# Optimization experiments

Measured on AMD Instinct MI355X. Metric: run time of the kernel, lower is better.

## Reference

```python
import jax, jax.numpy as jnp
import numpy as np

CONTEXT_LENGTH = 4096
INPUT_LENGTH = 1024
N_EMBED = 512
HEAD_SIZE = 64
BATCH = 8


def _prefix_causal_mask(T):
    # A=ones(IL,IL), B=zeros(IL,non), C=ones(non,IL), D=tril(non,non)
    il = INPUT_LENGTH
    non = CONTEXT_LENGTH - il
    top = jnp.concatenate([jnp.ones((il, il)), jnp.zeros((il, non))], axis=1)
    bot = jnp.concatenate([jnp.ones((non, il)), jnp.tril(jnp.ones((non, non)))], axis=1)
    E = jnp.concatenate([top, bot], axis=0)
    return E[:T, :T]


def setup_inputs() -> dict:
    key = jax.random.key(0)
    kx, kq, kk, kv = jax.random.split(key, 4)
    scale = N_EMBED ** -0.5
    return {
        "x": jax.random.normal(kx, (BATCH, CONTEXT_LENGTH, N_EMBED), dtype=jnp.float32),
        "Wq": jax.random.normal(kq, (N_EMBED, HEAD_SIZE), dtype=jnp.float32) * scale,
        "Wk": jax.random.normal(kk, (N_EMBED, HEAD_SIZE), dtype=jnp.float32) * scale,
        "Wv": jax.random.normal(kv, (N_EMBED, HEAD_SIZE), dtype=jnp.float32) * scale,
    }


def reference(x, Wq, Wk, Wv):
    B, T, C = x.shape
    q = x @ Wq  # [B,T,h]
    k = x @ Wk  # [B,T,h]
    v = x @ Wv  # [B,T,h]
    # NOTE: original scales by C**-0.5 with C = n_embed (not head_size)
    wei = jnp.einsum("bth,bsh->bts", q, k) * (C ** -0.5)  # [B,T,T]
    mask = _prefix_causal_mask(T)  # [T,T], 1 = visible
    wei = jnp.where(mask == 0, jnp.float32(-jnp.inf), wei)
    wei = jax.nn.softmax(wei, axis=-1)
    # dropout p=0.0 (eval): identity
    return jnp.einsum("bts,bsh->bth", wei, v)  # [B,T,h]
```

## Files before the change

kernel.cpp:

```cpp
#include <hip/hip_runtime.h>
#include <hip/hip_bf16.h>


typedef short short8 __attribute__((ext_vector_type(8)));
typedef float floatx4 __attribute__((ext_vector_type(4)));

static __device__ __forceinline__ unsigned short f2b(float f) {
  unsigned u = __float_as_uint(f);
  unsigned r = (u + 0x7fffu + ((u >> 16) & 1u)) >> 16;
  return (unsigned short)r;
}

static __device__ __forceinline__ unsigned pkbf(float lo, float hi) {
  __hip_bfloat162 t = __float22bfloat162_rn(make_float2(lo, hi));
  unsigned d;
  __builtin_memcpy(&d, &t, 4);
  return d;
}

union S8U {
  short8 s;
  unsigned u[4];
};

__global__ __launch_bounds__(256) void wtrans(
    const float* __restrict__ Wq, const float* __restrict__ Wk,
    const float* __restrict__ Wv, unsigned short* __restrict__ Wtf) {
  int o = blockIdx.x * 256 + threadIdx.x;
  int e = o & 7;
  int ln = (o >> 3) & 63;
  int jg = o >> 9;
  int ks = jg / 12;
  int j = jg % 12;
  int m = j >> 2;
  int n = (j & 3) * 16 + (ln & 15);
  int k = ks * 32 + (ln >> 4) * 8 + e;
  const float* W = (m == 0) ? Wq : (m == 1) ? Wk : Wv;
  Wtf[o] = f2b(W[k * 64 + n]);
}

__global__ __launch_bounds__(256, 2) void proj(
    const float* __restrict__ x, const unsigned short* __restrict__ Wtf,
    unsigned short* __restrict__ q, unsigned short* __restrict__ Kf,
    unsigned short* __restrict__ Vf) {
  __shared__ float Xs[2][64][36];
  __shared__ unsigned short Tl[64][72];

  const int tid = threadIdx.x;
  const int lane = tid & 63;
  const int w = tid >> 6;
  const int u = lane & 15;
  const int qd = lane >> 4;
  const int bx = blockIdx.x;
  const int g0 = bx * 64;
  const int b = bx >> 6;
  const int kt = bx & 63;

  const int srow = tid >> 3;
  const int sc4 = (tid & 7) * 4;

  floatx4 r0 = *reinterpret_cast<const floatx4*>(&x[(size_t)(g0 + srow) * 512 + sc4]);
  floatx4 r1 = *reinterpret_cast<const floatx4*>(&x[(size_t)(g0 + 32 + srow) * 512 + sc4]);
  *reinterpret_cast<floatx4*>(&Xs[0][srow][sc4]) = r0;
  *reinterpret_cast<floatx4*>(&Xs[0][32 + srow][sc4]) = r1;

  floatx4 acc[12];
#pragma unroll
  for (int j = 0; j < 12; ++j) acc[j] = (floatx4)0.0f;

  for (int ks = 0; ks < 16; ++ks) {
    if (ks < 15) {
      r0 = *reinterpret_cast<const floatx4*>(&x[(size_t)(g0 + srow) * 512 + (ks + 1) * 32 + sc4]);
      r1 = *reinterpret_cast<const floatx4*>(&x[(size_t)(g0 + 32 + srow) * 512 + (ks + 1) * 32 + sc4]);
    }
    __syncthreads();
    floatx4 a0 = *reinterpret_cast<const floatx4*>(&Xs[ks & 1][w * 16 + u][qd * 8]);
    floatx4 a1 = *reinterpret_cast<const floatx4*>(&Xs[ks & 1][w * 16 + u][qd * 8 + 4]);
    S8U a;
    a.u[0] = pkbf(a0[0], a0[1]);
    a.u[1] = pkbf(a0[2], a0[3]);
    a.u[2] = pkbf(a1[0], a1[1]);
    a.u[3] = pkbf(a1[2], a1[3]);
#pragma unroll
    for (int j = 0; j < 12; ++j) {
      short8 bfr = *reinterpret_cast<const short8*>(&Wtf[(size_t)(ks * 12 + j) * 512 + lane * 8]);
      acc[j] = __builtin_amdgcn_mfma_f32_16x16x32_bf16(a.s, bfr, acc[j], 0, 0, 0);
    }
    if (ks < 15) {
      *reinterpret_cast<floatx4*>(&Xs[(ks + 1) & 1][srow][sc4]) = r0;
      *reinterpret_cast<floatx4*>(&Xs[(ks + 1) & 1][32 + srow][sc4]) = r1;
    }
  }

#pragma unroll
  for (int j = 0; j < 4; ++j)
#pragma unroll
    for (int r = 0; r < 4; ++r)
      Tl[w * 16 + qd * 4 + r][j * 16 + u] = f2b(acc[j][r]);
  __syncthreads();
  {
    int row = tid >> 2, c0 = (tid & 3) * 16;
    short8 t0 = *reinterpret_cast<const short8*>(&Tl[row][c0]);
    short8 t1 = *reinterpret_cast<const short8*>(&Tl[row][c0 + 8]);
    *reinterpret_cast<short8*>(&q[(size_t)(g0 + row) * 64 + c0]) = t0;
    *reinterpret_cast<short8*>(&q[(size_t)(g0 + row) * 64 + c0 + 8]) = t1;
  }
  __syncthreads();

#pragma unroll
  for (int j = 0; j < 4; ++j)
#pragma unroll
    for (int r = 0; r < 4; ++r)
      Tl[w * 16 + qd * 4 + r][j * 16 + u] = f2b(acc[4 + j][r]);
  __syncthreads();
  {
    unsigned short* kfb = Kf + ((size_t)(b * 64 + kt)) * 4096;
#pragma unroll
    for (int f = w * 2; f < w * 2 + 2; ++f) {
      int kh = f >> 2, sb = f & 3;
      short8 v = *reinterpret_cast<const short8*>(&Tl[sb * 16 + u][kh * 32 + qd * 8]);
      *reinterpret_cast<short8*>(&kfb[(size_t)f * 512 + lane * 8]) = v;
    }
  }
  __syncthreads();

#pragma unroll
  for (int j = 0; j < 4; ++j)
#pragma unroll
    for (int r = 0; r < 4; ++r)
      Tl[j * 16 + u][w * 16 + qd * 4 + r] = f2b(acc[8 + j][r]);
  __syncthreads();
  {
    unsigned short* vfb = Vf + ((size_t)(b * 64 + kt)) * 4096;
#pragma unroll
    for (int f = w * 2; f < w * 2 + 2; ++f) {
      int sp = f >> 2, mb = f & 3;
      short8 v = *reinterpret_cast<const short8*>(&Tl[mb * 16 + u][sp * 32 + qd * 8]);
      *reinterpret_cast<short8*>(&vfb[(size_t)f * 512 + lane * 8]) = v;
    }
  }
}

__global__ __launch_bounds__(256, 2) void attn(
    const unsigned short* __restrict__ q, const unsigned short* __restrict__ Kf,
    const unsigned short* __restrict__ Vf, float* __restrict__ out) {
  __shared__ unsigned Pb[4][4][64][4];
  __shared__ float OcA[64][68];
  __shared__ float OcB[64][68];
  __shared__ float Lc[4][64];

  const int tid = threadIdx.x;
  const int lane = tid & 63;
  const int w = tid >> 6;
  const int u = lane & 15;
  const int qd = lane >> 4;

  const int bx = blockIdx.x;
  const int b = bx & 7;
  const int i = bx >> 3;
  const int qt = (i < 32) ? i : (95 - i);
  const int g0 = qt * 64;

  const unsigned short* qp = q + (size_t)b * 4096 * 64;
  const unsigned short* kfp = Kf + (size_t)b * 64 * 4096;
  const unsigned short* vfp = Vf + (size_t)b * 64 * 4096;

  short8 qB[4][2];
#pragma unroll
  for (int nb = 0; nb < 4; ++nb)
#pragma unroll
    for (int kh = 0; kh < 2; ++kh)
      qB[nb][kh] = *reinterpret_cast<const short8*>(
          &qp[(size_t)(g0 + nb * 16 + u) * 64 + kh * 32 + qd * 8]);

  floatx4 OT[4][4];
#pragma unroll
  for (int mb = 0; mb < 4; ++mb)
#pragma unroll
    for (int nb = 0; nb < 4; ++nb) OT[mb][nb] = (floatx4)0.0f;
  float L[4] = {0.f, 0.f, 0.f, 0.f};

  const float cexp = 0.04419417382415922f * 1.4426950408889634f;
  const int ktmax = (qt < 16) ? 15 : qt;

  for (int kt = w; kt <= ktmax; kt += 4) {
    const unsigned short* kb = kfp + (size_t)kt * 4096;
    const unsigned short* vb = vfp + (size_t)kt * 4096;
    short8 kA[8];
#pragma unroll
    for (int f = 0; f < 8; ++f)
      kA[f] = *reinterpret_cast<const short8*>(&kb[(size_t)f * 512 + lane * 8]);
    const bool diag = (qt >= 16) && (kt == qt);

#pragma unroll
    for (int sp = 0; sp < 2; ++sp) {
      short8 vA[4];
#pragma unroll
      for (int mb = 0; mb < 4; ++mb)
        vA[mb] = *reinterpret_cast<const short8*>(
            &vb[(size_t)(sp * 4 + mb) * 512 + lane * 8]);

      floatx4 ST[2][4];
#pragma unroll
      for (int sbb = 0; sbb < 2; ++sbb)
#pragma unroll
        for (int nb = 0; nb < 4; ++nb) ST[sbb][nb] = (floatx4)0.0f;
#pragma unroll
      for (int kh = 0; kh < 2; ++kh)
#pragma unroll
        for (int sbb = 0; sbb < 2; ++sbb)
#pragma unroll
          for (int nb = 0; nb < 4; ++nb)
            ST[sbb][nb] = __builtin_amdgcn_mfma_f32_16x16x32_bf16(
                kA[kh * 4 + sp * 2 + sbb], qB[nb][kh], ST[sbb][nb], 0, 0, 0);

      if (diag) {
#pragma unroll
        for (int sbb = 0; sbb < 2; ++sbb)
#pragma unroll
          for (int nb = 0; nb < 4; ++nb)
#pragma unroll
            for (int r = 0; r < 4; ++r) {
              int sl = (sp * 2 + sbb) * 16 + qd * 4 + r;
              int qr = nb * 16 + u;
              if (sl > qr) ST[sbb][nb][r] = -__builtin_inff();
            }
      }

#pragma unroll
      for (int sbb = 0; sbb < 2; ++sbb)
#pragma unroll
        for (int nb = 0; nb < 4; ++nb) {
#pragma unroll
          for (int r = 0; r < 4; ++r)
            ST[sbb][nb][r] = __builtin_amdgcn_exp2f(ST[sbb][nb][r] * cexp);
          L[nb] += (ST[sbb][nb][0] + ST[sbb][nb][1]) + (ST[sbb][nb][2] + ST[sbb][nb][3]);
          unsigned lo = pkbf(ST[sbb][nb][0], ST[sbb][nb][1]);
          unsigned hi = pkbf(ST[sbb][nb][2], ST[sbb][nb][3]);
          int dl = (sbb * 2 + (qd >> 1)) * 16 + u;
          int d0 = (qd & 1) * 2;
          *reinterpret_cast<uint2*>(&Pb[w][nb][dl][d0]) = make_uint2(lo, hi);
        }

#pragma unroll
      for (int nb = 0; nb < 4; ++nb) {
        short8 pB = *reinterpret_cast<const short8*>(&Pb[w][nb][lane][0]);
#pragma unroll
        for (int mb = 0; mb < 4; ++mb)
          OT[mb][nb] = __builtin_amdgcn_mfma_f32_16x16x32_bf16(vA[mb], pB, OT[mb][nb], 0, 0, 0);
      }
    }
  }

#pragma unroll
  for (int nb = 0; nb < 4; ++nb) {
    L[nb] += __shfl_xor(L[nb], 16);
    L[nb] += __shfl_xor(L[nb], 32);
  }
  if (lane < 16) {
#pragma unroll
    for (int nb = 0; nb < 4; ++nb) Lc[w][nb * 16 + lane] = L[nb];
  }

  if (w == 1) {
#pragma unroll
    for (int mb = 0; mb < 4; ++mb)
#pragma unroll
      for (int nb = 0; nb < 4; ++nb)
        *reinterpret_cast<floatx4*>(&OcA[nb * 16 + u][mb * 16 + qd * 4]) = OT[mb][nb];
  }
  if (w == 3) {
#pragma unroll
    for (int mb = 0; mb < 4; ++mb)
#pragma unroll
      for (int nb = 0; nb < 4; ++nb)
        *reinterpret_cast<floatx4*>(&OcB[nb * 16 + u][mb * 16 + qd * 4]) = OT[mb][nb];
  }
  __syncthreads();
  if (w == 0) {
#pragma unroll
    for (int mb = 0; mb < 4; ++mb)
#pragma unroll
      for (int nb = 0; nb < 4; ++nb)
        OT[mb][nb] += *reinterpret_cast<const floatx4*>(&OcA[nb * 16 + u][mb * 16 + qd * 4]);
  }
  if (w == 2) {
#pragma unroll
    for (int mb = 0; mb < 4; ++mb)
#pragma unroll
      for (int nb = 0; nb < 4; ++nb) {
        OT[mb][nb] += *reinterpret_cast<const floatx4*>(&OcB[nb * 16 + u][mb * 16 + qd * 4]);
        *reinterpret_cast<floatx4*>(&OcB[nb * 16 + u][mb * 16 + qd * 4]) = OT[mb][nb];
      }
  }
  __syncthreads();
  if (w == 0) {
#pragma unroll
    for (int mb = 0; mb < 4; ++mb)
#pragma unroll
      for (int nb = 0; nb < 4; ++nb) {
        OT[mb][nb] += *reinterpret_cast<const floatx4*>(&OcB[nb * 16 + u][mb * 16 + qd * 4]);
        *reinterpret_cast<floatx4*>(&OcA[nb * 16 + u][mb * 16 + qd * 4]) = OT[mb][nb];
      }
  }
  __syncthreads();

  {
    int qr = tid >> 2;
    int h0 = (tid & 3) * 16;
    float Ltot = (Lc[0][qr] + Lc[1][qr]) + (Lc[2][qr] + Lc[3][qr]);
    float inv = 1.0f / Ltot;
    float* op = out + ((size_t)b * 4096 + g0 + qr) * 64 + h0;
#pragma unroll
    for (int c = 0; c < 4; ++c) {
      floatx4 v = *reinterpret_cast<const floatx4*>(&OcA[qr][h0 + c * 4]);
      v *= inv;
      *reinterpret_cast<floatx4*>(&op[c * 4]) = v;
    }
  }
}

extern "C" void kernel_launch(void* const* d_in, const int* in_sizes, int n_in,
                              void* d_out, int out_size, void* d_ws, size_t ws_size,
                              hipStream_t stream) {
  const float* x  = (const float*)d_in[0];
  const float* Wq = (const float*)d_in[1];
  const float* Wk = (const float*)d_in[2];
  const float* Wv = (const float*)d_in[3];

  unsigned short* ws = (unsigned short*)d_ws;
  unsigned short* Wtf = ws;
  unsigned short* qb = ws + 131072;
  unsigned short* kf = qb + 2097152;
  unsigned short* vf = kf + 2097152;

  wtrans<<<384, 256, 0, stream>>>(Wq, Wk, Wv, Wtf);
  proj<<<512, 256, 0, stream>>>(x, Wtf, qb, kf, vf);
  attn<<<512, 256, 0, stream>>>(qb, kf, vf, (float*)d_out);
}
```

Measured before the change: 147.9 us.

## Split projection K-dimension across wave pairs and double proj grid

The projection kernel now processes 32 rows per block instead of 64 and launches twice as many blocks. Within a block, pairs of waves split the 512-wide reduction into even and odd K-steps and merge their partial sums through shared memory. Each wave loads x straight from global memory rather than through a double-buffered LDS tile. The goal is more parallelism and occupancy in proj, at the cost of scattered 2-byte global stores for the q/K/V output layouts.

```diff
diff --git a/kernel.cpp b/kernel.cpp
--- a/kernel.cpp
+++ b/kernel.cpp
@@ -39,105 +39,84 @@
   Wtf[o] = f2b(W[k * 64 + n]);
 }
 
-__global__ __launch_bounds__(256, 2) void proj(
+__global__ __launch_bounds__(256, 3) void proj(
     const float* __restrict__ x, const unsigned short* __restrict__ Wtf,
     unsigned short* __restrict__ q, unsigned short* __restrict__ Kf,
     unsigned short* __restrict__ Vf) {
-  __shared__ float Xs[2][64][36];
-  __shared__ unsigned short Tl[64][72];
+  __shared__ float Cc[2][12][16][17];
 
   const int tid = threadIdx.x;
   const int lane = tid & 63;
   const int w = tid >> 6;
   const int u = lane & 15;
   const int qd = lane >> 4;
-  const int bx = blockIdx.x;
-  const int g0 = bx * 64;
-  const int b = bx >> 6;
-  const int kt = bx & 63;
-
-  const int srow = tid >> 3;
-  const int sc4 = (tid & 7) * 4;
-
-  floatx4 r0 = *reinterpret_cast<const floatx4*>(&x[(size_t)(g0 + srow) * 512 + sc4]);
-  floatx4 r1 = *reinterpret_cast<const floatx4*>(&x[(size_t)(g0 + 32 + srow) * 512 + sc4]);
-  *reinterpret_cast<floatx4*>(&Xs[0][srow][sc4]) = r0;
-  *reinterpret_cast<floatx4*>(&Xs[0][32 + srow][sc4]) = r1;
+  const int pr = w >> 1;
+  const int p = w & 1;
+  const int g0 = blockIdx.x * 32;
 
   floatx4 acc[12];
 #pragma unroll
   for (int j = 0; j < 12; ++j) acc[j] = (floatx4)0.0f;
 
-  for (int ks = 0; ks < 16; ++ks) {
-    if (ks < 15) {
-      r0 = *reinterpret_cast<const floatx4*>(&x[(size_t)(g0 + srow) * 512 + (ks + 1) * 32 + sc4]);
-      r1 = *reinterpret_cast<const floatx4*>(&x[(size_t)(g0 + 32 + srow) * 512 + (ks + 1) * 32 + sc4]);
-    }
-    __syncthreads();
-    floatx4 a0 = *reinterpret_cast<const floatx4*>(&Xs[ks & 1][w * 16 + u][qd * 8]);
-    floatx4 a1 = *reinterpret_cast<const floatx4*>(&Xs[ks & 1][w * 16 + u][qd * 8 + 4]);
+  const float* xr = x + (size_t)(g0 + pr * 16 + u) * 512;
+
+  for (int it = 0; it < 8; ++it) {
+    const int ks = p + it * 2;
+    floatx4 x0 = *reinterpret_cast<const floatx4*>(&xr[ks * 32 + qd * 8]);
+    floatx4 x1 = *reinterpret_cast<const floatx4*>(&xr[ks * 32 + qd * 8 + 4]);
     S8U a;
-    a.u[0] = pkbf(a0[0], a0[1]);
-    a.u[1] = pkbf(a0[2], a0[3]);
-    a.u[2] = pkbf(a1[0], a1[1]);
-    a.u[3] = pkbf(a1[2], a1[3]);
+    a.u[0] = pkbf(x0[0], x0[1]);
+    a.u[1] = pkbf(x0[2], x0[3]);
+    a.u[2] = pkbf(x1[0], x1[1]);
+    a.u[3] = pkbf(x1[2], x1[3]);
 #pragma unroll
     for (int j = 0; j < 12; ++j) {
       short8 bfr = *reinterpret_cast<const short8*>(&Wtf[(size_t)(ks * 12 + j) * 512 + lane * 8]);
       acc[j] = __builtin_amdgcn_mfma_f32_16x16x32_bf16(a.s, bfr, acc[j], 0, 0, 0);
     }
-    if (ks < 15) {
-      *reinterpret_cast<floatx4*>(&Xs[(ks + 1) & 1][srow][sc4]) = r0;
-      *reinterpret_cast<floatx4*>(&Xs[(ks + 1) & 1][32 + srow][sc4]) = r1;
-    }
-  }
-
-#pragma unroll
-  for (int j = 0; j < 4; ++j)
-#pragma unroll
-    for (int r = 0; r < 4; ++r)
-      Tl[w * 16 + qd * 4 + r][j * 16 + u] = f2b(acc[j][r]);
+  }
+
+  if (p == 1) {
+#pragma unroll
+    for (int j = 0; j < 12; ++j)
+#pragma unroll
+      for (int r = 0; r < 4; ++r)
+        Cc[pr][j][qd * 4 + r][u] = acc[j][r];
+  }
   __syncthreads();
-  {
-    int row = tid >> 2, c0 = (tid & 3) * 16;
-    short8 t0 = *reinterpret_cast<const short8*>(&Tl[row][c0]);
-    short8 t1 = *reinterpret_cast<const short8*>(&Tl[row][c0 + 8]);
-    *reinterpret_cast<short8*>(&q[(size_t)(g0 + row) * 64 + c0]) = t0;
-    *reinterpret_cast<short8*>(&q[(size_t)(g0 + row) * 64 + c0 + 8]) = t1;
-  }
-  __syncthreads();
-
-#pragma unroll
-  for (int j = 0; j < 4; ++j)
-#pragma unroll
-    for (int r = 0; r < 4; ++r)
-      Tl[w * 16 + qd * 4 + r][j * 16 + u] = f2b(acc[4 + j][r]);
-  __syncthreads();
-  {
+  if (p == 0) {
+#pragma unroll
+    for (int j = 0; j < 12; ++j)
+#pragma unroll
+      for (int r = 0; r < 4; ++r)
+        acc[j][r] += Cc[pr][j][qd * 4 + r][u];
+
+    const int rbase = g0 + pr * 16;
+    const int b = rbase >> 12;
+    const int t = rbase & 4095;
+    const int kt = t >> 6;
+    const int sb = ((blockIdx.x & 1) << 1) + pr;
+    const int sp = blockIdx.x & 1;
     unsigned short* kfb = Kf + ((size_t)(b * 64 + kt)) * 4096;
-#pragma unroll
-    for (int f = w * 2; f < w * 2 + 2; ++f) {
-      int kh = f >> 2, sb = f & 3;
-      short8 v = *reinterpret_cast<const short8*>(&Tl[sb * 16 + u][kh * 32 + qd * 8]);
-      *reinterpret_cast<short8*>(&kfb[(size_t)f * 512 + lane * 8]) = v;
-    }
-  }
-  __syncthreads();
-
-#pragma unroll
-  for (int j = 0; j < 4; ++j)
-#pragma unroll
-    for (int r = 0; r < 4; ++r)
-      Tl[j * 16 + u][w * 16 + qd * 4 + r] = f2b(acc[8 + j][r]);
-  __syncthreads();
-  {
     unsigned short* vfb = Vf + ((size_t)(b * 64 + kt)) * 4096;
-#pragma unroll
-    for (int f = w * 2; f < w * 2 + 2; ++f) {
-      int sp = f >> 2, mb = f & 3;
-      short8 v = *reinterpret_cast<const short8*>(&Tl[mb * 16 + u][sp * 32 + qd * 8]);
-      *reinterpret_cast<short8*>(&vfb[(size_t)f * 512 + lane * 8]) = v;
-    }
+
+#pragma unroll
+    for (int j = 0; j < 4; ++j)
+#pragma unroll
+      for (int r = 0; r < 4; ++r) {
+        q[(size_t)(rbase + qd * 4 + r) * 64 + j * 16 + u] = f2b(acc[j][r]);
+        {
+          int kh = j >> 1;
+          int qd_f = ((j & 1) << 1) + (u >> 3);
+          kfb[(size_t)(kh * 4 + sb) * 512 + (qd_f * 16 + (qd * 4 + r)) * 8 + (u & 7)] =
+              f2b(acc[4 + j][r]);
+        }
+        {
+          int qd_f = pr * 2 + (qd >> 1);
+          int e = ((qd & 1) << 2) + r;
+          vfb[(size_t)(sp * 4 + j) * 512 + (qd_f * 16 + u) * 8 + e] = f2b(acc[8 + j][r]);
+        }
+      }
   }
 }
 
@@ -335,6 +314,6 @@
   unsigned short* vf = kf + 2097152;
 
   wtrans<<<384, 256, 0, stream>>>(Wq, Wk, Wv, Wtf);
-  proj<<<512, 256, 0, stream>>>(x, Wtf, qb, kf, vf);
+  proj<<<1024, 256, 0, stream>>>(x, Wtf, qb, kf, vf);
   attn<<<512, 256, 0, stream>>>(qb, kf, vf, (float*)d_out);
 }
```

Measured after the change: 146.9 us. No clear change (-0.7%).
